# Performance work log

Measured on AMD Instinct MI355X. Metric: run time of the kernel, lower is better.

## Reference

```python
import math
import jax, jax.numpy as jnp
import numpy as np

D = 1024        # latent_dim
H = 16          # num latent heads
HD = D // H     # head dim = 64
T_EMB = 9       # max(diffusion_steps+1, 2)
CLIP = 1.0      # latent_update_clip
LN_EPS = 1e-5


def layer_norm(x, g, b):
    m = jnp.mean(x, axis=-1, keepdims=True)
    v = jnp.mean(jnp.square(x - m), axis=-1, keepdims=True)
    return (x - m) * jax.lax.rsqrt(v + LN_EPS) * g + b


def setup_inputs() -> dict:
    key = jax.random.key(0)
    ks = jax.random.split(key, 10)
    B, S = 64, 64
    s = 0.02
    return {
        "latents": jax.random.normal(ks[0], (B, S, D), jnp.float32),
        "t_table": jax.random.normal(ks[1], (T_EMB, D), jnp.float32) * s,
        "attn_g": jnp.ones((D,), jnp.float32),
        "attn_b": jnp.zeros((D,), jnp.float32),
        "ffn_g": jnp.ones((D,), jnp.float32),
        "ffn_b": jnp.zeros((D,), jnp.float32),
        "Wq": jax.random.normal(ks[2], (D, D), jnp.float32) * s,
        "Wk": jax.random.normal(ks[3], (D, D), jnp.float32) * s,
        "Wv": jax.random.normal(ks[4], (D, D), jnp.float32) * s,
        "Wo": jax.random.normal(ks[5], (D, D), jnp.float32) * s,
        "Win": jax.random.normal(ks[6], (2 * D, D), jnp.float32) * s,
        "b_in": jnp.zeros((2 * D,), jnp.float32),
        "Wout": jax.random.normal(ks[7], (D, 2 * D), jnp.float32) * s,
        "b_out": jnp.zeros((D,), jnp.float32),
        "steps": 8,
    }


def _slot_attention(x, Wq, Wk, Wv, Wo):
    B, S, _ = x.shape
    scale = 1.0 / math.sqrt(HD)
    # torch Linear: y = x @ W.T ; weights stored (out, in)
    q = (x @ Wq.T).reshape(B, S, H, HD)
    k = (x @ Wk.T).reshape(B, S, H, HD)
    v = (x @ Wv.T).reshape(B, S, H, HD)
    scores = jnp.einsum("bqhd,bkhd->bhqk", q, k) * scale
    probs = jax.nn.softmax(scores, axis=-1)
    out = jnp.einsum("bhqk,bkhd->bqhd", probs, v).reshape(B, S, D)
    return out @ Wo.T


def reference(latents, t_table, attn_g, attn_b, ffn_g, ffn_b,
              Wq, Wk, Wv, Wo, Win, b_in, Wout, b_out, steps):
    h = latents
    for step in range(steps):
        step_id = min(step, T_EMB - 1)
        t_emb = t_table[step_id][None, None, :]          # [1,1,D]
        attn_update = _slot_attention(layer_norm(h + t_emb, attn_g, attn_b),
                                      Wq, Wk, Wv, Wo)
        ffn_in = layer_norm(h + t_emb + attn_update, ffn_g, ffn_b)
        ffn_update = jax.nn.silu(ffn_in @ Win.T + b_in) @ Wout.T + b_out
        update = attn_update + ffn_update
        unorm = jnp.maximum(jnp.linalg.norm(update, axis=-1, keepdims=True), 1e-6)
        update = update * jnp.minimum(CLIP / unorm, 1.0)
        h = h + update / steps
    return h
```

## Files before the change

### kernel.cpp

```cpp
#include <hip/hip_runtime.h>
#include <hip/hip_bf16.h>

typedef __attribute__((ext_vector_type(8))) short bf16x8;
typedef __attribute__((ext_vector_type(4))) float f32x4;
typedef __attribute__((ext_vector_type(4))) int i32x4;

static __device__ __forceinline__ short f2bf(float f) {
    __hip_bfloat16 h = __float2bfloat16(f);
    return __builtin_bit_cast(short, h);
}
static __device__ __forceinline__ float bf2f(short s) {
    unsigned u = ((unsigned)(unsigned short)s) << 16;
    return __builtin_bit_cast(float, u);
}

static __device__ __forceinline__ void gload_lds16(const short* g, short* l) {
    __builtin_amdgcn_global_load_lds((const __attribute__((address_space(1))) void*)g,
                                     (__attribute__((address_space(3))) void*)l, 16, 0, 0);
}

__global__ void convert_kernel(const float* __restrict__ src, short* __restrict__ dst, int n) {
    for (int i = blockIdx.x * blockDim.x + threadIdx.x; i < n; i += gridDim.x * blockDim.x)
        dst[i] = f2bf(src[i]);
}

__global__ void copy_kernel(const float* __restrict__ src, float* __restrict__ dst, int n) {
    for (int i = blockIdx.x * blockDim.x + threadIdx.x; i < n; i += gridDim.x * blockDim.x)
        dst[i] = src[i];
}

__global__ __launch_bounds__(256) void ln_kernel(
    const float* __restrict__ hsrc, const float* __restrict__ trow,
    const short* __restrict__ add,
    const float* __restrict__ g, const float* __restrict__ bb,
    short* __restrict__ out)
{
    const int row = blockIdx.x;
    const int tid = threadIdx.x;
    const int lane = tid & 63;
    const int wid = tid >> 6;
    __shared__ float red[4];
    const float* hr = hsrc + (size_t)row * 1024;
    float x[4];
    float s = 0.f;
    #pragma unroll
    for (int i = 0; i < 4; ++i) {
        int c = tid + i * 256;
        float v = hr[c] + trow[c];
        if (add) v += bf2f(add[(size_t)row * 1024 + c]);
        x[i] = v; s += v;
    }
    #pragma unroll
    for (int o = 32; o >= 1; o >>= 1) s += __shfl_xor(s, o, 64);
    if (lane == 0) red[wid] = s;
    __syncthreads();
    float mean = (red[0] + red[1] + red[2] + red[3]) * (1.0f / 1024.0f);
    __syncthreads();
    float s2 = 0.f;
    #pragma unroll
    for (int i = 0; i < 4; ++i) { float d = x[i] - mean; s2 += d * d; }
    #pragma unroll
    for (int o = 32; o >= 1; o >>= 1) s2 += __shfl_xor(s2, o, 64);
    if (lane == 0) red[wid] = s2;
    __syncthreads();
    float var = (red[0] + red[1] + red[2] + red[3]) * (1.0f / 1024.0f);
    float rstd = rsqrtf(var + 1e-5f);
    #pragma unroll
    for (int i = 0; i < 4; ++i) {
        int c = tid + i * 256;
        out[(size_t)row * 1024 + c] = f2bf((x[i] - mean) * rstd * g[c] + bb[c]);
    }
}

__global__ __launch_bounds__(256) void clipln_kernel(
    const short* __restrict__ upd, float* __restrict__ h,
    const float* __restrict__ trow,
    const float* __restrict__ g, const float* __restrict__ bb,
    short* __restrict__ out)
{
    const int row = blockIdx.x;
    const int tid = threadIdx.x;
    const int lane = tid & 63;
    const int wid = tid >> 6;
    __shared__ float red[4];
    const short* ur = upd + (size_t)row * 1024;
    float u[4], hn[4];
    float s = 0.f;
    #pragma unroll
    for (int i = 0; i < 4; ++i) { u[i] = bf2f(ur[tid + i * 256]); s += u[i] * u[i]; }
    #pragma unroll
    for (int o = 32; o >= 1; o >>= 1) s += __shfl_xor(s, o, 64);
    if (lane == 0) red[wid] = s;
    __syncthreads();
    float nrm = sqrtf(red[0] + red[1] + red[2] + red[3]);
    float scale = fminf(1.0f / fmaxf(nrm, 1e-6f), 1.0f) * 0.125f;
    __syncthreads();
    float sm = 0.f;
    #pragma unroll
    for (int i = 0; i < 4; ++i) {
        int c = tid + i * 256;
        hn[i] = h[(size_t)row * 1024 + c] + u[i] * scale;
        h[(size_t)row * 1024 + c] = hn[i];
        hn[i] += trow[c];
        sm += hn[i];
    }
    #pragma unroll
    for (int o = 32; o >= 1; o >>= 1) sm += __shfl_xor(sm, o, 64);
    if (lane == 0) red[wid] = sm;
    __syncthreads();
    float mean = (red[0] + red[1] + red[2] + red[3]) * (1.0f / 1024.0f);
    __syncthreads();
    float s2 = 0.f;
    #pragma unroll
    for (int i = 0; i < 4; ++i) { float d = hn[i] - mean; s2 += d * d; }
    #pragma unroll
    for (int o = 32; o >= 1; o >>= 1) s2 += __shfl_xor(s2, o, 64);
    if (lane == 0) red[wid] = s2;
    __syncthreads();
    float var = (red[0] + red[1] + red[2] + red[3]) * (1.0f / 1024.0f);
    float rstd = rsqrtf(var + 1e-5f);
    #pragma unroll
    for (int i = 0; i < 4; ++i) {
        int c = tid + i * 256;
        out[(size_t)row * 1024 + c] = f2bf((hn[i] - mean) * rstd * g[c] + bb[c]);
    }
}

template<int BM, int ACT, int ADD, int BIAS>
__global__ __launch_bounds__(512) void gemm_kernel(
    const short* __restrict__ A, const short* __restrict__ B,
    const float* __restrict__ bias, const short* __restrict__ addsrc,
    short* __restrict__ Cout, int M, int N, int K)
{
    const int nwg = gridDim.x * gridDim.y;
    const int orig = blockIdx.y * gridDim.x + blockIdx.x;
    const int swzid = (orig & 7) * (nwg >> 3) + (orig >> 3);
    const int bn = (swzid % gridDim.x) * 128;
    const int bm = (swzid / gridDim.x) * BM;

    __shared__ __align__(16) short As[2][BM * 64];
    __shared__ __align__(16) short Bs[2][128 * 64];
    const int tid = threadIdx.x;
    const int lane = tid & 63;
    const int wid = tid >> 6;
    const int l15 = lane & 15;
    const int l4 = lane >> 4;

    constexpr int MF = 2;
    constexpr int NF = (BM == 128) ? 4 : 2;
    const int rowbase = (BM == 128) ? (wid >> 1) * 32 : (wid >> 2) * 32;
    const int colbase = (BM == 128) ? (wid & 1) * 64 : (wid & 3) * 32;

    constexpr int ALOADS = BM * 8 / 512;
    constexpr int LOADS = ALOADS + 2;

    f32x4 acc[MF][NF];
    #pragma unroll
    for (int m = 0; m < MF; ++m)
        #pragma unroll
        for (int n = 0; n < NF; ++n)
            acc[m][n] = (f32x4)(0.f);

    auto stage = [&](int k0, int buf) {
        #pragma unroll
        for (int i = 0; i < ALOADS; ++i) {
            int slot = i * 512 + tid;
            int row = slot >> 3;
            int colb = (slot & 7) * 16;
            int swz = (row & 7) << 4;
            const short* g = A + (size_t)(bm + row) * K + k0 + ((colb ^ swz) >> 1);
            gload_lds16(g, (short*)((char*)As[buf] + slot * 16));
        }
        #pragma unroll
        for (int i = 0; i < 2; ++i) {
            int slot = i * 512 + tid;
            int row = slot >> 3;
            int colb = (slot & 7) * 16;
            int swz = (row & 7) << 4;
            const short* g = B + (size_t)(bn + row) * K + k0 + ((colb ^ swz) >> 1);
            gload_lds16(g, (short*)((char*)Bs[buf] + slot * 16));
        }
    };

    stage(0, 0);
    const int nt = K >> 6;
    for (int t = 0; t < nt; ++t) {
        const int cur = t & 1;
        if (t + 1 < nt) {
            stage((t + 1) << 6, cur ^ 1);
            if constexpr (LOADS == 4) asm volatile("s_waitcnt vmcnt(4)" ::: "memory");
            else                      asm volatile("s_waitcnt vmcnt(3)" ::: "memory");
        } else {
            asm volatile("s_waitcnt vmcnt(0)" ::: "memory");
        }
        __builtin_amdgcn_s_barrier();
        #pragma unroll
        for (int ks = 0; ks < 2; ++ks) {
            int kb = ks * 64 + l4 * 16;
            bf16x8 a[MF], b[NF];
            #pragma unroll
            for (int m = 0; m < MF; ++m) {
                int row = rowbase + m * 16 + l15;
                a[m] = *(const bf16x8*)((const char*)As[cur] + row * 128 + (kb ^ ((row & 7) << 4)));
            }
            #pragma unroll
            for (int n = 0; n < NF; ++n) {
                int row = colbase + n * 16 + l15;
                b[n] = *(const bf16x8*)((const char*)Bs[cur] + row * 128 + (kb ^ ((row & 7) << 4)));
            }
            #pragma unroll
            for (int m = 0; m < MF; ++m)
                #pragma unroll
                for (int n = 0; n < NF; ++n)
                    acc[m][n] = __builtin_amdgcn_mfma_f32_16x16x32_bf16(a[m], b[n], acc[m][n], 0, 0, 0);
        }
        __builtin_amdgcn_s_barrier();
    }

    #pragma unroll
    for (int m = 0; m < MF; ++m) {
        int row = bm + rowbase + m * 16 + l4 * 4;
        #pragma unroll
        for (int n = 0; n < NF; ++n) {
            int col = bn + colbase + n * 16 + l15;
            float bv = BIAS ? bias[col] : 0.f;
            #pragma unroll
            for (int r = 0; r < 4; ++r) {
                float v = acc[m][n][r] + bv;
                if (ACT) v = v / (1.f + __expf(-v));
                if (ADD) v += bf2f(addsrc[(size_t)(row + r) * N + col]);
                Cout[(size_t)(row + r) * N + col] = f2bf(v);
            }
        }
    }
}

__global__ __launch_bounds__(256) void attn_kernel(
    const short* __restrict__ qkv,
    short* __restrict__ ctx)
{
    const int blk = blockIdx.x;
    const int b = blk >> 4, hh = blk & 15;
    const int bs0 = b * 64;
    __shared__ __align__(16) short qs[64 * 64];
    __shared__ __align__(16) short ks_[64 * 64];
    __shared__ __align__(16) short vt[64 * 64];
    __shared__ __align__(16) short ps[64 * 64];
    const int tid = threadIdx.x;
    const int lane = tid & 63;
    const int wid = tid >> 6;
    const int l15 = lane & 15;
    const int l4 = lane >> 4;

    #pragma unroll
    for (int i = 0; i < 2; ++i) {
        int slot = i * 256 + tid;
        int row = slot >> 3;
        int colb = (slot & 7) * 16;
        int swz = (row & 7) << 4;
        const short* gq = qkv + (size_t)(bs0 + row) * 3072 + hh * 64 + (slot & 7) * 8;
        *(i32x4*)((char*)qs + row * 128 + (colb ^ swz)) = *(const i32x4*)gq;
        const short* gk = qkv + (size_t)(bs0 + row) * 3072 + 1024 + hh * 64 + (slot & 7) * 8;
        *(i32x4*)((char*)ks_ + row * 128 + (colb ^ swz)) = *(const i32x4*)gk;
        const short* gv = qkv + (size_t)(bs0 + row) * 3072 + 2048 + hh * 64 + (slot & 7) * 8;
        i32x4 vv = *(const i32x4*)gv;
        const short* ve = (const short*)&vv;
        #pragma unroll
        for (int j = 0; j < 8; ++j) {
            int d = (slot & 7) * 8 + j;
            *(short*)((char*)vt + d * 128 + ((row * 2) ^ ((d & 7) << 4))) = ve[j];
        }
    }
    __syncthreads();

    f32x4 sc[4];
    #pragma unroll
    for (int n = 0; n < 4; ++n) sc[n] = (f32x4)(0.f);
    #pragma unroll
    for (int ksz = 0; ksz < 2; ++ksz) {
        int kb = ksz * 64 + l4 * 16;
        int arow = wid * 16 + l15;
        bf16x8 af = *(const bf16x8*)((const char*)qs + arow * 128 + (kb ^ ((arow & 7) << 4)));
        #pragma unroll
        for (int n = 0; n < 4; ++n) {
            int brow = n * 16 + l15;
            bf16x8 bf = *(const bf16x8*)((const char*)ks_ + brow * 128 + (kb ^ ((brow & 7) << 4)));
            sc[n] = __builtin_amdgcn_mfma_f32_16x16x32_bf16(af, bf, sc[n], 0, 0, 0);
        }
    }
    float sm[4];
    #pragma unroll
    for (int r = 0; r < 4; ++r) {
        float m = -1e30f;
        #pragma unroll
        for (int n = 0; n < 4; ++n) { sc[n][r] *= 0.125f; m = fmaxf(m, sc[n][r]); }
        #pragma unroll
        for (int o = 1; o < 16; o <<= 1) m = fmaxf(m, __shfl_xor(m, o, 64));
        float s = 0.f;
        #pragma unroll
        for (int n = 0; n < 4; ++n) { sc[n][r] = __expf(sc[n][r] - m); s += sc[n][r]; }
        #pragma unroll
        for (int o = 1; o < 16; o <<= 1) s += __shfl_xor(s, o, 64);
        sm[r] = 1.f / s;
    }
    #pragma unroll
    for (int n = 0; n < 4; ++n)
        #pragma unroll
        for (int r = 0; r < 4; ++r) {
            int row = wid * 16 + l4 * 4 + r;
            int col = n * 16 + l15;
            *(short*)((char*)ps + row * 128 + ((col * 2) ^ ((row & 7) << 4))) = f2bf(sc[n][r] * sm[r]);
        }
    __syncthreads();

    f32x4 o[4];
    #pragma unroll
    for (int n = 0; n < 4; ++n) o[n] = (f32x4)(0.f);
    #pragma unroll
    for (int ksz = 0; ksz < 2; ++ksz) {
        int kb = ksz * 64 + l4 * 16;
        int arow = wid * 16 + l15;
        bf16x8 af = *(const bf16x8*)((const char*)ps + arow * 128 + (kb ^ ((arow & 7) << 4)));
        #pragma unroll
        for (int n = 0; n < 4; ++n) {
            int vrow = n * 16 + l15;
            bf16x8 bf = *(const bf16x8*)((const char*)vt + vrow * 128 + (kb ^ ((vrow & 7) << 4)));
            o[n] = __builtin_amdgcn_mfma_f32_16x16x32_bf16(af, bf, o[n], 0, 0, 0);
        }
    }
    #pragma unroll
    for (int n = 0; n < 4; ++n)
        #pragma unroll
        for (int r = 0; r < 4; ++r) {
            int row = wid * 16 + l4 * 4 + r;
            int col = n * 16 + l15;
            ctx[(size_t)(bs0 + row) * 1024 + hh * 64 + col] = f2bf(o[n][r]);
        }
}

__global__ __launch_bounds__(256) void clip_kernel(const short* __restrict__ upd, float* __restrict__ h) {
    const int row = blockIdx.x;
    const int tid = threadIdx.x;
    const int lane = tid & 63;
    const int wid = tid >> 6;
    __shared__ float red[4];
    const short* ur = upd + (size_t)row * 1024;
    float x[4];
    float s = 0.f;
    #pragma unroll
    for (int i = 0; i < 4; ++i) { x[i] = bf2f(ur[tid + i * 256]); s += x[i] * x[i]; }
    #pragma unroll
    for (int o = 32; o >= 1; o >>= 1) s += __shfl_xor(s, o, 64);
    if (lane == 0) red[wid] = s;
    __syncthreads();
    float nrm = sqrtf(red[0] + red[1] + red[2] + red[3]);
    float unorm = fmaxf(nrm, 1e-6f);
    float scale = fminf(1.0f / unorm, 1.0f) * 0.125f;
    #pragma unroll
    for (int i = 0; i < 4; ++i) {
        int c = tid + i * 256;
        h[(size_t)row * 1024 + c] += x[i] * scale;
    }
}

extern "C" void kernel_launch(void* const* d_in, const int* in_sizes, int n_in,
                              void* d_out, int out_size, void* d_ws, size_t ws_size,
                              hipStream_t stream) {
    const float* latents = (const float*)d_in[0];
    const float* t_table = (const float*)d_in[1];
    const float* attn_g  = (const float*)d_in[2];
    const float* attn_b  = (const float*)d_in[3];
    const float* ffn_g   = (const float*)d_in[4];
    const float* ffn_b   = (const float*)d_in[5];
    const float* Wq      = (const float*)d_in[6];
    const float* Wk      = (const float*)d_in[7];
    const float* Wv      = (const float*)d_in[8];
    const float* Wo      = (const float*)d_in[9];
    const float* Win     = (const float*)d_in[10];
    const float* b_in    = (const float*)d_in[11];
    const float* Wout    = (const float*)d_in[12];
    const float* b_out   = (const float*)d_in[13];

    char* ws = (char*)d_ws;
    size_t off = 0;
    auto alloc = [&](size_t bytes) { char* p = ws + off; off += (bytes + 255) & ~(size_t)255; return p; };
    short* wQKV = (short*)alloc((size_t)3072 * 1024 * 2);
    short* wO   = (short*)alloc((size_t)1024 * 1024 * 2);
    short* wIn  = (short*)alloc((size_t)2048 * 1024 * 2);
    short* wOut = (short*)alloc((size_t)1024 * 2048 * 2);
    short* xln  = (short*)alloc((size_t)4096 * 1024 * 2);
    short* qkv  = (short*)alloc((size_t)4096 * 3072 * 2);
    short* hidden = qkv;
    short* ctx  = (short*)alloc((size_t)4096 * 1024 * 2);
    short* au   = (short*)alloc((size_t)4096 * 1024 * 2);
    short* upd  = (short*)alloc((size_t)4096 * 1024 * 2);

    float* h = (float*)d_out;

    convert_kernel<<<1024, 256, 0, stream>>>(Wq,   wQKV,               1024 * 1024);
    convert_kernel<<<1024, 256, 0, stream>>>(Wk,   wQKV + 1024 * 1024, 1024 * 1024);
    convert_kernel<<<1024, 256, 0, stream>>>(Wv,   wQKV + 2048 * 1024, 1024 * 1024);
    convert_kernel<<<1024, 256, 0, stream>>>(Wo,   wO,                 1024 * 1024);
    convert_kernel<<<2048, 256, 0, stream>>>(Win,  wIn,                2048 * 1024);
    convert_kernel<<<2048, 256, 0, stream>>>(Wout, wOut,               2048 * 1024);
    copy_kernel<<<2048, 256, 0, stream>>>(latents, h, 4096 * 1024);

    ln_kernel<<<4096, 256, 0, stream>>>(h, t_table, nullptr, attn_g, attn_b, xln);

    for (int step = 0; step < 8; ++step) {
        const float* trow = t_table + (size_t)step * 1024;
        gemm_kernel<128, 0, 0, 0><<<dim3(24, 32), 512, 0, stream>>>(xln, wQKV, nullptr, nullptr, qkv, 4096, 3072, 1024);
        attn_kernel<<<1024, 256, 0, stream>>>(qkv, ctx);
        gemm_kernel<64, 0, 0, 0><<<dim3(8, 64), 512, 0, stream>>>(ctx, wO, nullptr, nullptr, au, 4096, 1024, 1024);
        ln_kernel<<<4096, 256, 0, stream>>>(h, trow, au, ffn_g, ffn_b, xln);
        gemm_kernel<128, 1, 0, 1><<<dim3(16, 32), 512, 0, stream>>>(xln, wIn, b_in, nullptr, hidden, 4096, 2048, 1024);
        gemm_kernel<64, 0, 1, 1><<<dim3(8, 64), 512, 0, stream>>>(hidden, wOut, b_out, au, upd, 4096, 1024, 2048);
        if (step < 7) {
            clipln_kernel<<<4096, 256, 0, stream>>>(upd, h, t_table + (size_t)(step + 1) * 1024,
                                                    attn_g, attn_b, xln);
        } else {
            clip_kernel<<<4096, 256, 0, stream>>>(upd, h);
        }
    }
}
```

Before: 1.049 ms.

## Use 256x128 single-buffered GEMM for QKV/FFN-in and 128x128 tiles elsewhere

```diff
diff --git a/kernel.cpp b/kernel.cpp
--- a/kernel.cpp
+++ b/kernel.cpp
@@ -126,8 +126,100 @@
     }
 }
 
-template<int BM, int ACT, int ADD, int BIAS>
-__global__ __launch_bounds__(512) void gemm_kernel(
+template<int ACT, int BIAS>
+__global__ __launch_bounds__(512) void gemm_big(
+    const short* __restrict__ A, const short* __restrict__ B,
+    const float* __restrict__ bias, short* __restrict__ Cout,
+    int M, int N, int K)
+{
+    const int nwg = gridDim.x * gridDim.y;
+    const int orig = blockIdx.y * gridDim.x + blockIdx.x;
+    const int swzid = (orig & 7) * (nwg >> 3) + (orig >> 3);
+    const int bn = (swzid % gridDim.x) * 128;
+    const int bm = (swzid / gridDim.x) * 256;
+
+    __shared__ __align__(16) short As[256 * 64];
+    __shared__ __align__(16) short Bs[128 * 64];
+    const int tid = threadIdx.x;
+    const int lane = tid & 63;
+    const int wid = tid >> 6;
+    const int l15 = lane & 15;
+    const int l4 = lane >> 4;
+    const int rowbase = (wid >> 1) * 64;
+    const int colbase = (wid & 1) * 64;
+
+    f32x4 acc[4][4];
+    #pragma unroll
+    for (int m = 0; m < 4; ++m)
+        #pragma unroll
+        for (int n = 0; n < 4; ++n)
+            acc[m][n] = (f32x4)(0.f);
+
+    const int nt = K >> 6;
+    for (int t = 0; t < nt; ++t) {
+        const int k0 = t << 6;
+        #pragma unroll
+        for (int i = 0; i < 4; ++i) {
+            int slot = i * 512 + tid;
+            int row = slot >> 3;
+            int colb = (slot & 7) * 16;
+            int swz = (row & 7) << 4;
+            const short* g = A + (size_t)(bm + row) * K + k0 + ((colb ^ swz) >> 1);
+            gload_lds16(g, (short*)((char*)As + slot * 16));
+        }
+        #pragma unroll
+        for (int i = 0; i < 2; ++i) {
+            int slot = i * 512 + tid;
+            int row = slot >> 3;
+            int colb = (slot & 7) * 16;
+            int swz = (row & 7) << 4;
+            const short* g = B + (size_t)(bn + row) * K + k0 + ((colb ^ swz) >> 1);
+            gload_lds16(g, (short*)((char*)Bs + slot * 16));
+        }
+        asm volatile("s_waitcnt vmcnt(0)" ::: "memory");
+        __syncthreads();
+        #pragma unroll
+        for (int ks = 0; ks < 2; ++ks) {
+            int kb = ks * 64 + l4 * 16;
+            bf16x8 a[4], b[4];
+            #pragma unroll
+            for (int m = 0; m < 4; ++m) {
+                int row = rowbase + m * 16 + l15;
+                a[m] = *(const bf16x8*)((const char*)As + row * 128 + (kb ^ ((row & 7) << 4)));
+            }
+            #pragma unroll
+            for (int n = 0; n < 4; ++n) {
+                int row = colbase + n * 16 + l15;
+                b[n] = *(const bf16x8*)((const char*)Bs + row * 128 + (kb ^ ((row & 7) << 4)));
+            }
+            #pragma unroll
+            for (int m = 0; m < 4; ++m)
+                #pragma unroll
+                for (int n = 0; n < 4; ++n)
+                    acc[m][n] = __builtin_amdgcn_mfma_f32_16x16x32_bf16(a[m], b[n], acc[m][n], 0, 0, 0);
+        }
+        __syncthreads();
+    }
+
+    #pragma unroll
+    for (int m = 0; m < 4; ++m) {
+        int row = bm + rowbase + m * 16 + l4 * 4;
+        #pragma unroll
+        for (int n = 0; n < 4; ++n) {
+            int col = bn + colbase + n * 16 + l15;
+            float bv = BIAS ? bias[col] : 0.f;
+            #pragma unroll
+            for (int r = 0; r < 4; ++r) {
+                float v = acc[m][n][r] + bv;
+                if (ACT) v = v / (1.f + __expf(-v));
+                Cout[(size_t)(row + r) * N + col] = f2bf(v);
+            }
+        }
+    }
+}
+
+template<int ACT, int ADD, int BIAS>
+__global__ __launch_bounds__(512) void gemm_std(
     const short* __restrict__ A, const short* __restrict__ B,
     const float* __restrict__ bias, const short* __restrict__ addsrc,
     short* __restrict__ Cout, int M, int N, int K)
@@ -136,34 +228,28 @@
     const int orig = blockIdx.y * gridDim.x + blockIdx.x;
     const int swzid = (orig & 7) * (nwg >> 3) + (orig >> 3);
     const int bn = (swzid % gridDim.x) * 128;
-    const int bm = (swzid / gridDim.x) * BM;
-
-    __shared__ __align__(16) short As[2][BM * 64];
+    const int bm = (swzid / gridDim.x) * 128;
+
+    __shared__ __align__(16) short As[2][128 * 64];
     __shared__ __align__(16) short Bs[2][128 * 64];
     const int tid = threadIdx.x;
     const int lane = tid & 63;
     const int wid = tid >> 6;
     const int l15 = lane & 15;
     const int l4 = lane >> 4;
-
-    constexpr int MF = 2;
-    constexpr int NF = (BM == 128) ? 4 : 2;
-    const int rowbase = (BM == 128) ? (wid >> 1) * 32 : (wid >> 2) * 32;
-    const int colbase = (BM == 128) ? (wid & 1) * 64 : (wid & 3) * 32;
-
-    constexpr int ALOADS = BM * 8 / 512;
-    constexpr int LOADS = ALOADS + 2;
-
-    f32x4 acc[MF][NF];
-    #pragma unroll
-    for (int m = 0; m < MF; ++m)
-        #pragma unroll
-        for (int n = 0; n < NF; ++n)
+    const int rowbase = (wid >> 1) * 32;
+    const int colbase = (wid & 1) * 64;
+
+    f32x4 acc[2][4];
+    #pragma unroll
+    for (int m = 0; m < 2; ++m)
+        #pragma unroll
+        for (int n = 0; n < 4; ++n)
             acc[m][n] = (f32x4)(0.f);
 
     auto stage = [&](int k0, int buf) {
         #pragma unroll
-        for (int i = 0; i < ALOADS; ++i) {
+        for (int i = 0; i < 2; ++i) {
             int slot = i * 512 + tid;
             int row = slot >> 3;
             int colb = (slot & 7) * 16;
@@ -188,8 +274,7 @@
         const int cur = t & 1;
         if (t + 1 < nt) {
             stage((t + 1) << 6, cur ^ 1);
-            if constexpr (LOADS == 4) asm volatile("s_waitcnt vmcnt(4)" ::: "memory");
-            else                      asm volatile("s_waitcnt vmcnt(3)" ::: "memory");
+            asm volatile("s_waitcnt vmcnt(4)" ::: "memory");
         } else {
             asm volatile("s_waitcnt vmcnt(0)" ::: "memory");
         }
@@ -197,31 +282,31 @@
         #pragma unroll
         for (int ks = 0; ks < 2; ++ks) {
             int kb = ks * 64 + l4 * 16;
-            bf16x8 a[MF], b[NF];
-            #pragma unroll
-            for (int m = 0; m < MF; ++m) {
+            bf16x8 a[2], b[4];
+            #pragma unroll
+            for (int m = 0; m < 2; ++m) {
                 int row = rowbase + m * 16 + l15;
                 a[m] = *(const bf16x8*)((const char*)As[cur] + row * 128 + (kb ^ ((row & 7) << 4)));
             }
             #pragma unroll
-            for (int n = 0; n < NF; ++n) {
+            for (int n = 0; n < 4; ++n) {
                 int row = colbase + n * 16 + l15;
                 b[n] = *(const bf16x8*)((const char*)Bs[cur] + row * 128 + (kb ^ ((row & 7) << 4)));
             }
             #pragma unroll
-            for (int m = 0; m < MF; ++m)
+            for (int m = 0; m < 2; ++m)
                 #pragma unroll
-                for (int n = 0; n < NF; ++n)
+                for (int n = 0; n < 4; ++n)
                     acc[m][n] = __builtin_amdgcn_mfma_f32_16x16x32_bf16(a[m], b[n], acc[m][n], 0, 0, 0);
         }
         __builtin_amdgcn_s_barrier();
     }
 
     #pragma unroll
-    for (int m = 0; m < MF; ++m) {
+    for (int m = 0; m < 2; ++m) {
         int row = bm + rowbase + m * 16 + l4 * 4;
         #pragma unroll
-        for (int n = 0; n < NF; ++n) {
+        for (int n = 0; n < 4; ++n) {
             int col = bn + colbase + n * 16 + l15;
             float bv = BIAS ? bias[col] : 0.f;
             #pragma unroll
@@ -409,12 +494,12 @@
 
     for (int step = 0; step < 8; ++step) {
         const float* trow = t_table + (size_t)step * 1024;
-        gemm_kernel<128, 0, 0, 0><<<dim3(24, 32), 512, 0, stream>>>(xln, wQKV, nullptr, nullptr, qkv, 4096, 3072, 1024);
+        gemm_big<0, 0><<<dim3(24, 16), 512, 0, stream>>>(xln, wQKV, nullptr, qkv, 4096, 3072, 1024);
         attn_kernel<<<1024, 256, 0, stream>>>(qkv, ctx);
-        gemm_kernel<64, 0, 0, 0><<<dim3(8, 64), 512, 0, stream>>>(ctx, wO, nullptr, nullptr, au, 4096, 1024, 1024);
+        gemm_std<0, 0, 0><<<dim3(8, 32), 512, 0, stream>>>(ctx, wO, nullptr, nullptr, au, 4096, 1024, 1024);
         ln_kernel<<<4096, 256, 0, stream>>>(h, trow, au, ffn_g, ffn_b, xln);
-        gemm_kernel<128, 1, 0, 1><<<dim3(16, 32), 512, 0, stream>>>(xln, wIn, b_in, nullptr, hidden, 4096, 2048, 1024);
-        gemm_kernel<64, 0, 1, 1><<<dim3(8, 64), 512, 0, stream>>>(hidden, wOut, b_out, au, upd, 4096, 1024, 2048);
+        gemm_big<1, 1><<<dim3(16, 16), 512, 0, stream>>>(xln, wIn, b_in, hidden, 4096, 2048, 1024);
+        gemm_std<0, 1, 1><<<dim3(8, 32), 512, 0, stream>>>(hidden, wOut, b_out, au, upd, 4096, 1024, 2048);
         if (step < 7) {
             clipln_kernel<<<4096, 256, 0, stream>>>(upd, h, t_table + (size_t)(step + 1) * 1024,
                                                     attn_g, attn_b, xln);
```

New measurement: 1.103 ms. 5.2% more time.

## Enlarge GEMM warp tiles to 64x64 per wave and fuse setup kernels

Applied to the files above, without the earlier changes.

```diff
diff --git a/kernel.cpp b/kernel.cpp
--- a/kernel.cpp
+++ b/kernel.cpp
@@ -19,14 +19,67 @@
                                      (__attribute__((address_space(3))) void*)l, 16, 0, 0);
 }
 
-__global__ void convert_kernel(const float* __restrict__ src, short* __restrict__ dst, int n) {
-    for (int i = blockIdx.x * blockDim.x + threadIdx.x; i < n; i += gridDim.x * blockDim.x)
-        dst[i] = f2bf(src[i]);
-}
-
-__global__ void copy_kernel(const float* __restrict__ src, float* __restrict__ dst, int n) {
-    for (int i = blockIdx.x * blockDim.x + threadIdx.x; i < n; i += gridDim.x * blockDim.x)
-        dst[i] = src[i];
+__global__ void convert_all_kernel(
+    const float* __restrict__ Wq, const float* __restrict__ Wk, const float* __restrict__ Wv,
+    const float* __restrict__ Wo, const float* __restrict__ Win, const float* __restrict__ Wout,
+    short* __restrict__ wQKV, short* __restrict__ wO, short* __restrict__ wIn, short* __restrict__ wOut)
+{
+    const int M1 = 1024 * 1024;
+    for (int i = blockIdx.x * blockDim.x + threadIdx.x; i < 8 * M1; i += gridDim.x * blockDim.x) {
+        if (i < 3 * M1) {
+            float v = (i < M1) ? Wq[i] : (i < 2 * M1) ? Wk[i - M1] : Wv[i - 2 * M1];
+            wQKV[i] = f2bf(v);
+        } else if (i < 4 * M1) {
+            wO[i - 3 * M1] = f2bf(Wo[i - 3 * M1]);
+        } else if (i < 6 * M1) {
+            wIn[i - 4 * M1] = f2bf(Win[i - 4 * M1]);
+        } else {
+            wOut[i - 6 * M1] = f2bf(Wout[i - 6 * M1]);
+        }
+    }
+}
+
+__global__ __launch_bounds__(256) void first_ln_kernel(
+    const float* __restrict__ latents, float* __restrict__ h,
+    const float* __restrict__ trow,
+    const float* __restrict__ g, const float* __restrict__ bb,
+    short* __restrict__ out)
+{
+    const int row = blockIdx.x;
+    const int tid = threadIdx.x;
+    const int lane = tid & 63;
+    const int wid = tid >> 6;
+    __shared__ float red[4];
+    const float* hr = latents + (size_t)row * 1024;
+    float x[4];
+    float s = 0.f;
+    #pragma unroll
+    for (int i = 0; i < 4; ++i) {
+        int c = tid + i * 256;
+        float hv = hr[c];
+        h[(size_t)row * 1024 + c] = hv;
+        x[i] = hv + trow[c]; s += x[i];
+    }
+    #pragma unroll
+    for (int o = 32; o >= 1; o >>= 1) s += __shfl_xor(s, o, 64);
+    if (lane == 0) red[wid] = s;
+    __syncthreads();
+    float mean = (red[0] + red[1] + red[2] + red[3]) * (1.0f / 1024.0f);
+    __syncthreads();
+    float s2 = 0.f;
+    #pragma unroll
+    for (int i = 0; i < 4; ++i) { float d = x[i] - mean; s2 += d * d; }
+    #pragma unroll
+    for (int o = 32; o >= 1; o >>= 1) s2 += __shfl_xor(s2, o, 64);
+    if (lane == 0) red[wid] = s2;
+    __syncthreads();
+    float var = (red[0] + red[1] + red[2] + red[3]) * (1.0f / 1024.0f);
+    float rstd = rsqrtf(var + 1e-5f);
+    #pragma unroll
+    for (int i = 0; i < 4; ++i) {
+        int c = tid + i * 256;
+        out[(size_t)row * 1024 + c] = f2bf((x[i] - mean) * rstd * g[c] + bb[c]);
+    }
 }
 
 __global__ __launch_bounds__(256) void ln_kernel(
@@ -126,8 +179,8 @@
     }
 }
 
-template<int BM, int ACT, int ADD, int BIAS>
-__global__ __launch_bounds__(512) void gemm_kernel(
+template<int BM, int BN, int NT, int ACT, int ADD, int BIAS>
+__global__ __launch_bounds__(NT) void gemm_t(
     const short* __restrict__ A, const short* __restrict__ B,
     const float* __restrict__ bias, const short* __restrict__ addsrc,
     short* __restrict__ Cout, int M, int N, int K)
@@ -135,45 +188,49 @@
     const int nwg = gridDim.x * gridDim.y;
     const int orig = blockIdx.y * gridDim.x + blockIdx.x;
     const int swzid = (orig & 7) * (nwg >> 3) + (orig >> 3);
-    const int bn = (swzid % gridDim.x) * 128;
+    const int bn = (swzid % gridDim.x) * BN;
     const int bm = (swzid / gridDim.x) * BM;
 
     __shared__ __align__(16) short As[2][BM * 64];
-    __shared__ __align__(16) short Bs[2][128 * 64];
+    __shared__ __align__(16) short Bs[2][BN * 64];
     const int tid = threadIdx.x;
     const int lane = tid & 63;
     const int wid = tid >> 6;
     const int l15 = lane & 15;
     const int l4 = lane >> 4;
 
-    constexpr int MF = 2;
-    constexpr int NF = (BM == 128) ? 4 : 2;
-    const int rowbase = (BM == 128) ? (wid >> 1) * 32 : (wid >> 2) * 32;
-    const int colbase = (BM == 128) ? (wid & 1) * 64 : (wid & 3) * 32;
-
-    constexpr int ALOADS = BM * 8 / 512;
-    constexpr int LOADS = ALOADS + 2;
-
-    f32x4 acc[MF][NF];
-    #pragma unroll
-    for (int m = 0; m < MF; ++m)
-        #pragma unroll
-        for (int n = 0; n < NF; ++n)
+    constexpr int WN = BN / 64;
+    const int rowbase = (wid / WN) * 64;
+    const int colbase = (wid % WN) * 64;
+
+    constexpr int SA = BM * 8;
+    constexpr int SB = BN * 8;
+    constexpr int AIT = (SA + NT - 1) / NT;
+    constexpr int BIT = SB / NT;
+    constexpr int LW = SA / NT + SB / NT;
+
+    f32x4 acc[4][4];
+    #pragma unroll
+    for (int m = 0; m < 4; ++m)
+        #pragma unroll
+        for (int n = 0; n < 4; ++n)
             acc[m][n] = (f32x4)(0.f);
 
     auto stage = [&](int k0, int buf) {
         #pragma unroll
-        for (int i = 0; i < ALOADS; ++i) {
-            int slot = i * 512 + tid;
-            int row = slot >> 3;
-            int colb = (slot & 7) * 16;
-            int swz = (row & 7) << 4;
-            const short* g = A + (size_t)(bm + row) * K + k0 + ((colb ^ swz) >> 1);
-            gload_lds16(g, (short*)((char*)As[buf] + slot * 16));
-        }
-        #pragma unroll
-        for (int i = 0; i < 2; ++i) {
-            int slot = i * 512 + tid;
+        for (int i = 0; i < AIT; ++i) {
+            int slot = i * NT + tid;
+            if (AIT * NT == SA || slot < SA) {
+                int row = slot >> 3;
+                int colb = (slot & 7) * 16;
+                int swz = (row & 7) << 4;
+                const short* g = A + (size_t)(bm + row) * K + k0 + ((colb ^ swz) >> 1);
+                gload_lds16(g, (short*)((char*)As[buf] + slot * 16));
+            }
+        }
+        #pragma unroll
+        for (int i = 0; i < BIT; ++i) {
+            int slot = i * NT + tid;
             int row = slot >> 3;
             int colb = (slot & 7) * 16;
             int swz = (row & 7) << 4;
@@ -188,8 +245,10 @@
         const int cur = t & 1;
         if (t + 1 < nt) {
             stage((t + 1) << 6, cur ^ 1);
-            if constexpr (LOADS == 4) asm volatile("s_waitcnt vmcnt(4)" ::: "memory");
-            else                      asm volatile("s_waitcnt vmcnt(3)" ::: "memory");
+            if constexpr (LW == 5)      asm volatile("s_waitcnt vmcnt(5)" ::: "memory");
+            else if constexpr (LW == 6) asm volatile("s_waitcnt vmcnt(6)" ::: "memory");
+            else if constexpr (LW == 8) asm volatile("s_waitcnt vmcnt(8)" ::: "memory");
+            else                        asm volatile("s_waitcnt vmcnt(4)" ::: "memory");
         } else {
             asm volatile("s_waitcnt vmcnt(0)" ::: "memory");
         }
@@ -197,31 +256,31 @@
         #pragma unroll
         for (int ks = 0; ks < 2; ++ks) {
             int kb = ks * 64 + l4 * 16;
-            bf16x8 a[MF], b[NF];
+            bf16x8 a[4], b[4];
             #pragma unroll
-            for (int m = 0; m < MF; ++m) {
+            for (int m = 0; m < 4; ++m) {
                 int row = rowbase + m * 16 + l15;
                 a[m] = *(const bf16x8*)((const char*)As[cur] + row * 128 + (kb ^ ((row & 7) << 4)));
             }
             #pragma unroll
-            for (int n = 0; n < NF; ++n) {
+            for (int n = 0; n < 4; ++n) {
                 int row = colbase + n * 16 + l15;
                 b[n] = *(const bf16x8*)((const char*)Bs[cur] + row * 128 + (kb ^ ((row & 7) << 4)));
             }
             #pragma unroll
-            for (int m = 0; m < MF; ++m)
+            for (int m = 0; m < 4; ++m)
                 #pragma unroll
-                for (int n = 0; n < NF; ++n)
+                for (int n = 0; n < 4; ++n)
                     acc[m][n] = __builtin_amdgcn_mfma_f32_16x16x32_bf16(a[m], b[n], acc[m][n], 0, 0, 0);
         }
         __builtin_amdgcn_s_barrier();
     }
 
     #pragma unroll
-    for (int m = 0; m < MF; ++m) {
+    for (int m = 0; m < 4; ++m) {
         int row = bm + rowbase + m * 16 + l4 * 4;
         #pragma unroll
-        for (int n = 0; n < NF; ++n) {
+        for (int n = 0; n < 4; ++n) {
             int col = bn + colbase + n * 16 + l15;
             float bv = BIAS ? bias[col] : 0.f;
             #pragma unroll
@@ -397,24 +456,17 @@
 
     float* h = (float*)d_out;
 
-    convert_kernel<<<1024, 256, 0, stream>>>(Wq,   wQKV,               1024 * 1024);
-    convert_kernel<<<1024, 256, 0, stream>>>(Wk,   wQKV + 1024 * 1024, 1024 * 1024);
-    convert_kernel<<<1024, 256, 0, stream>>>(Wv,   wQKV + 2048 * 1024, 1024 * 1024);
-    convert_kernel<<<1024, 256, 0, stream>>>(Wo,   wO,                 1024 * 1024);
-    convert_kernel<<<2048, 256, 0, stream>>>(Win,  wIn,                2048 * 1024);
-    convert_kernel<<<2048, 256, 0, stream>>>(Wout, wOut,               2048 * 1024);
-    copy_kernel<<<2048, 256, 0, stream>>>(latents, h, 4096 * 1024);
-
-    ln_kernel<<<4096, 256, 0, stream>>>(h, t_table, nullptr, attn_g, attn_b, xln);
+    convert_all_kernel<<<2048, 256, 0, stream>>>(Wq, Wk, Wv, Wo, Win, Wout, wQKV, wO, wIn, wOut);
+    first_ln_kernel<<<4096, 256, 0, stream>>>(latents, h, t_table, attn_g, attn_b, xln);
 
     for (int step = 0; step < 8; ++step) {
         const float* trow = t_table + (size_t)step * 1024;
-        gemm_kernel<128, 0, 0, 0><<<dim3(24, 32), 512, 0, stream>>>(xln, wQKV, nullptr, nullptr, qkv, 4096, 3072, 1024);
+        gemm_t<128, 384, 768, 0, 0, 0><<<dim3(8, 32), 768, 0, stream>>>(xln, wQKV, nullptr, nullptr, qkv, 4096, 3072, 1024);
         attn_kernel<<<1024, 256, 0, stream>>>(qkv, ctx);
-        gemm_kernel<64, 0, 0, 0><<<dim3(8, 64), 512, 0, stream>>>(ctx, wO, nullptr, nullptr, au, 4096, 1024, 1024);
+        gemm_t<128, 128, 256, 0, 0, 0><<<dim3(8, 32), 256, 0, stream>>>(ctx, wO, nullptr, nullptr, au, 4096, 1024, 1024);
         ln_kernel<<<4096, 256, 0, stream>>>(h, trow, au, ffn_g, ffn_b, xln);
-        gemm_kernel<128, 1, 0, 1><<<dim3(16, 32), 512, 0, stream>>>(xln, wIn, b_in, nullptr, hidden, 4096, 2048, 1024);
-        gemm_kernel<64, 0, 1, 1><<<dim3(8, 64), 512, 0, stream>>>(hidden, wOut, b_out, au, upd, 4096, 1024, 2048);
+        gemm_t<128, 256, 512, 1, 0, 1><<<dim3(8, 32), 512, 0, stream>>>(xln, wIn, b_in, nullptr, hidden, 4096, 2048, 1024);
+        gemm_t<128, 128, 256, 0, 1, 1><<<dim3(8, 32), 256, 0, stream>>>(hidden, wOut, b_out, au, upd, 4096, 1024, 2048);
         if (step < 7) {
             clipln_kernel<<<4096, 256, 0, stream>>>(upd, h, t_table + (size_t)(step + 1) * 1024,
                                                     attn_g, attn_b, xln);
```

New measurement: 1.126 ms. +7.3%, slower.
